# Kernel tuning notes

Measured on AMD Instinct MI355X. Metric: run time of the kernel, lower is better.

The kernel has to match this reference:

```python
import jax, jax.numpy as jnp
import numpy as np

DIM_IN = 768
DIM_EMB = 512
DIM_ATTN = 384
N_EXPERTS = 13
TOP_K = 5
NUM_CLS = 2
K_INST = 100000  # instances per bag (WSI patches)


def setup_inputs() -> dict:
    key = jax.random.key(0)
    ks = jax.random.split(key, 10)
    s = 0.02  # weight init scale
    return {
        "X_tfl": jax.random.normal(ks[0], (1, N_EXPERTS, DIM_EMB), jnp.float32),
        "X": jax.random.normal(ks[1], (1, K_INST, DIM_IN), jnp.float32),
        # feat_proj: Linear(dim_in, dim_emb) + ReLU (end_with_fc=False, eval -> no dropout)
        "W_proj": (jax.random.normal(ks[2], (DIM_IN, DIM_EMB), jnp.float32) * s),
        "b_proj": jnp.zeros((DIM_EMB,), jnp.float32),
        # Attn_Net: Linear(L,D) -> Tanh -> Linear(D,1)
        "W_attn1": (jax.random.normal(ks[3], (DIM_EMB, DIM_ATTN), jnp.float32) * s),
        "b_attn1": jnp.zeros((DIM_ATTN,), jnp.float32),
        "W_attn2": (jax.random.normal(ks[4], (DIM_ATTN, 1), jnp.float32) * s),
        "b_attn2": jnp.zeros((1,), jnp.float32),
        # router: Linear(dim_emb, n_experts, bias=False)
        "W_router": (jax.random.normal(ks[5], (DIM_EMB, N_EXPERTS), jnp.float32) * s),
        # pred_head: Linear(dim_emb, num_cls)
        "W_pred": (jax.random.normal(ks[6], (DIM_EMB, NUM_CLS), jnp.float32) * s),
        "b_pred": jnp.zeros((NUM_CLS,), jnp.float32),
    }


def reference(X_tfl, X, W_proj, b_proj, W_attn1, b_attn1, W_attn2, b_attn2,
              W_router, W_pred, b_pred):
    # feat_proj (eval mode: dropout is identity)
    H = jax.nn.relu(jnp.einsum('bkc,cd->bkd', X, W_proj) + b_proj)  # [1,K,512]
    # attention pooling (Attn_Net): tanh MLP -> scalar score per instance
    scores = jnp.einsum('bkd,de->bke', jnp.tanh(H @ W_attn1 + b_attn1), W_attn2) + b_attn2  # [1,K,1]
    A = jax.nn.softmax(scores[..., 0], axis=-1)      # [1,K]
    M = jnp.einsum('bk,bkd->bd', A, H)               # [1,512] slide representation
    # router + top-k gating
    router_logits = M @ W_router                     # [1,13]
    probs = jax.nn.softmax(router_logits, axis=-1)
    weights, sel_idx = jax.lax.top_k(probs, TOP_K)   # [1,5], [1,5]
    # Identity experts: expert i output is X_tfl[0, i, :]; gather selected, weighted combine
    sel = X_tfl[0][sel_idx[0]]                       # [5,512]
    moe_output = jnp.sum(weights[0][:, None] * sel, axis=0)[None, :]  # [1,512]
    logit = moe_output @ W_pred + b_pred             # [1,2]
    return logit
```

## Files before the change

### kernel.cpp

```cpp
#include <hip/hip_runtime.h>
#include <hip/hip_bf16.h>

typedef __attribute__((ext_vector_type(8))) short short8_t;
typedef __attribute__((ext_vector_type(4))) float f32x4;
typedef __attribute__((ext_vector_type(4))) unsigned int u32x4;

#define KINST 100000
#define KPAD  100096
#define DIMIN 768
#define DIMEMB 512
#define DIMATTN 384

__device__ __forceinline__ unsigned short f2bf(float f) {
    unsigned int u = __builtin_bit_cast(unsigned int, f);
    u = u + 0x7FFFu + ((u >> 16) & 1u);
    return (unsigned short)(u >> 16);
}
__device__ __forceinline__ unsigned int packbf(float a, float b) {
    return (unsigned int)f2bf(a) | ((unsigned int)f2bf(b) << 16);
}
__device__ __forceinline__ float bf2f(unsigned short h) {
    unsigned int u = ((unsigned int)h) << 16;
    return __builtin_bit_cast(float, u);
}
__device__ __forceinline__ float fast_tanh(float x) {
    const float e2 = __expf(2.f * x);
    return (e2 - 1.f) * __builtin_amdgcn_rcpf(e2 + 1.f);
}
__device__ __forceinline__ void gll16(const unsigned short* g, unsigned short* l) {
    __builtin_amdgcn_global_load_lds(
        (const __attribute__((address_space(1))) unsigned int*)g,
        (__attribute__((address_space(3))) unsigned int*)l, 16, 0, 0);
}

__global__ __launch_bounds__(256) void k_prep(
    const float* __restrict__ Wproj, const float* __restrict__ W1,
    unsigned short* __restrict__ WpTt, unsigned short* __restrict__ W1Ts)
{
    const int idx = blockIdx.x * 256 + threadIdx.x;
    if (idx < 49152) {
        const int t = idx >> 11, r = idx & 2047;
        const int n = r >> 2, c = r & 3;
        short8_t v;
        #pragma unroll
        for (int e = 0; e < 8; ++e)
            v[e] = (short)f2bf(Wproj[(size_t)(t * 32 + c * 8 + e) * DIMEMB + n]);
        *(short8_t*)&WpTt[t * 16384 + n * 32 + c * 8] = v;
    } else {
        const int j = idx - 49152;
        const int t = j / 3072, r = j % 3072;
        const int c = r / 384, n = r % 384;
        short8_t v;
        #pragma unroll
        for (int e = 0; e < 8; ++e)
            v[e] = (short)f2bf(W1[(size_t)(t * 64 + c * 8 + e) * DIMATTN + n]);
        *(short8_t*)&W1Ts[t * 24576 + n * 64 + ((c ^ (n & 7)) << 3)] = v;
    }
}

__global__ __launch_bounds__(256, 2) void k_gemm1(
    const float* __restrict__ X,
    const unsigned short* __restrict__ WpTt,
    const float* __restrict__ bproj,
    unsigned short* __restrict__ H)
{
    __shared__ unsigned short As[2][2048];
    const int tid = threadIdx.x;
    const int lane = tid & 63, w = tid >> 6;
    const int g = lane >> 4, fr = lane & 15;
    const int brow = blockIdx.x * 64;

    const int arow = tid >> 2, aq4 = tid & 3;
    int agr = brow + arow; if (agr >= KINST) agr = KINST - 1;
    const float* xsrc = X + (size_t)agr * DIMIN + aq4 * 8;
    const int awoff = arow * 32 + ((aq4 ^ ((arow >> 1) & 3)) << 3);
    const int aro = (g ^ ((fr >> 1) & 3)) << 3;

    const unsigned short* gB = WpTt + (size_t)(w * 128 + fr) * 32 + g * 8;

    f32x4 acc[4][8] = {};
    short8_t Bf[2][8];
    float4 xva, xvb;

    {
        float4 xa = *(const float4*)(xsrc);
        float4 xb = *(const float4*)(xsrc + 4);
        #pragma unroll
        for (int j = 0; j < 8; ++j)
            Bf[0][j] = *(const short8_t*)(gB + j * 512);
        xva = *(const float4*)(xsrc + 32);
        xvb = *(const float4*)(xsrc + 36);
        u32x4 p;
        p[0] = packbf(xa.x, xa.y); p[1] = packbf(xa.z, xa.w);
        p[2] = packbf(xb.x, xb.y); p[3] = packbf(xb.z, xb.w);
        *(u32x4*)&As[0][awoff] = p;
    }
    asm volatile("s_waitcnt lgkmcnt(0)" ::: "memory");
    __builtin_amdgcn_sched_barrier(0);
    __builtin_amdgcn_s_barrier();
    __builtin_amdgcn_sched_barrier(0);

#define G1STEP(P, T)                                                           \
    {                                                                          \
        if ((T) < 23) {       \
            const unsigned short* gBt = gB + (size_t)((T) + 1) * 16384;        \
            _Pragma("unroll")                                                  \
            for (int j = 0; j < 8; ++j)                                        \
                Bf[(P) ^ 1][j] = *(const short8_t*)(gBt + j * 512);            \
        }                                                                      \
        short8_t af[4];                      \
        _Pragma("unroll")                                                      \
        for (int i = 0; i < 4; ++i)                                            \
            af[i] = *(const short8_t*)&As[P][(i * 16 + fr) * 32 + aro];        \
        if ((T) < 23) {                     \
            u32x4 p;                                                           \
            p[0] = packbf(xva.x, xva.y); p[1] = packbf(xva.z, xva.w);          \
            p[2] = packbf(xvb.x, xvb.y); p[3] = packbf(xvb.z, xvb.w);          \
            *(u32x4*)&As[(P) ^ 1][awoff] = p;                                  \
        }                                                                      \
        if ((T) < 22) {                   \
            xva = *(const float4*)(xsrc + ((T) + 2) * 32);                     \
            xvb = *(const float4*)(xsrc + ((T) + 2) * 32 + 4);                 \
        }                                                                      \
        asm volatile("s_waitcnt lgkmcnt(0)" ::: "memory");                     \
        __builtin_amdgcn_sched_barrier(0);                                     \
        __builtin_amdgcn_s_barrier();                                          \
        __builtin_amdgcn_sched_barrier(0);                                     \
        __builtin_amdgcn_s_setprio(1);                                        \
        _Pragma("unroll")                                                      \
        for (int j = 0; j < 8; ++j)                                            \
            _Pragma("unroll")                                                  \
            for (int i = 0; i < 4; ++i)                                        \
                acc[i][j] = __builtin_amdgcn_mfma_f32_16x16x32_bf16(           \
                    af[i], Bf[P][j], acc[i][j], 0, 0, 0);                      \
        __builtin_amdgcn_s_setprio(0);                                        \
    }

    for (int tt = 0; tt < 24; tt += 2) {
        G1STEP(0, tt);
        G1STEP(1, tt + 1);
    }
#undef G1STEP

    #pragma unroll
    for (int j = 0; j < 8; ++j) {
        const int col = w * 128 + j * 16 + fr;
        const float bias = bproj[col];
        const int tile = (col >> 6) << 6, cc = (col >> 3) & 7, lo = col & 7;
        #pragma unroll
        for (int i = 0; i < 4; ++i) {
            const int rb = brow + i * 16 + g * 4;
            #pragma unroll
            for (int r = 0; r < 4; ++r) {
                const int row = rb + r;
                const float v = fmaxf(acc[i][j][r] + bias, 0.f);
                H[(size_t)row * DIMEMB + tile + ((cc ^ (row & 7)) << 3) + lo] =
                    (row < KINST) ? f2bf(v) : (unsigned short)0;
            }
        }
    }
}

__global__ __launch_bounds__(256) void k_gemm2(
    const unsigned short* __restrict__ H,
    const unsigned short* __restrict__ W1Ts,
    const float* __restrict__ b1,
    const float* __restrict__ W2,
    float* __restrict__ Tpart)
{
    __shared__ unsigned short As[2][8192];
    __shared__ unsigned short Bs[2][8192];
    __shared__ float sred[2][128];
    const int tid = threadIdx.x;
    const int lane = tid & 63, w = tid >> 6;
    const int wr = w >> 1, wc = w & 1;
    const int g = lane >> 4, fr = lane & 15;
    const int cb = blockIdx.x;
    const int brow = blockIdx.y * 128;
    const int bcol = cb * 128;

    const unsigned short* gA = H + (size_t)(brow + w * 32 + (lane >> 3)) * DIMEMB + (lane & 7) * 8;
    const unsigned short* gB = W1Ts + (size_t)(bcol + w * 32 + (lane >> 3)) * 64 + (lane & 7) * 8;
    const int loff = w * 2048 + lane * 8;

    f32x4 acc[4][4] = {};

    #pragma unroll
    for (int q = 0; q < 4; ++q) {
        gll16(gA + q * 4096, &As[0][loff + q * 512]);
        gll16(gB + q * 512,  &Bs[0][loff + q * 512]);
    }
    __syncthreads();

    for (int t = 0; t < 8; ++t) {
        const int buf = t & 1;
        if (t < 7) {
            #pragma unroll
            for (int q = 0; q < 4; ++q) {
                gll16(gA + (t + 1) * 64 + q * 4096,           &As[buf ^ 1][loff + q * 512]);
                gll16(gB + (size_t)(t + 1) * 24576 + q * 512, &Bs[buf ^ 1][loff + q * 512]);
            }
        }
        __builtin_amdgcn_s_setprio(1);
        #pragma unroll
        for (int kk = 0; kk < 2; ++kk) {
            short8_t af[4];
            #pragma unroll
            for (int i = 0; i < 4; ++i) {
                const int row = wr * 64 + i * 16 + fr;
                af[i] = *(const short8_t*)&As[buf][row * 64 + (((kk * 4 + g) ^ (fr & 7)) << 3)];
            }
            #pragma unroll
            for (int j = 0; j < 4; ++j) {
                const int rowb = wc * 64 + j * 16 + fr;
                const short8_t bf = *(const short8_t*)&Bs[buf][rowb * 64 + (((kk * 4 + g) ^ (fr & 7)) << 3)];
                #pragma unroll
                for (int i = 0; i < 4; ++i)
                    acc[i][j] = __builtin_amdgcn_mfma_f32_16x16x32_bf16(af[i], bf, acc[i][j], 0, 0, 0);
            }
        }
        __builtin_amdgcn_s_setprio(0);
        if (t < 7) __syncthreads();
    }

    float ps[4][4] = {};
    #pragma unroll
    for (int j = 0; j < 4; ++j) {
        const int col = bcol + wc * 64 + j * 16 + fr;
        const float bb = b1[col], ww = W2[col];
        #pragma unroll
        for (int i = 0; i < 4; ++i)
            #pragma unroll
            for (int r = 0; r < 4; ++r)
                ps[i][r] += fast_tanh(acc[i][j][r] + bb) * ww;
    }
    #pragma unroll
    for (int off = 1; off < 16; off <<= 1)
        #pragma unroll
        for (int i = 0; i < 4; ++i)
            #pragma unroll
            for (int r = 0; r < 4; ++r)
                ps[i][r] += __shfl_xor(ps[i][r], off, 64);
    if (fr == 0) {
        #pragma unroll
        for (int i = 0; i < 4; ++i)
            #pragma unroll
            for (int r = 0; r < 4; ++r)
                sred[wc][wr * 64 + i * 16 + g * 4 + r] = ps[i][r];
    }
    __syncthreads();
    if (tid < 128)
        Tpart[(size_t)cb * KPAD + brow + tid] = sred[0][tid] + sred[1][tid];
}

__global__ __launch_bounds__(512) void k_poolE(
    const float* __restrict__ Tpart,
    const unsigned short* __restrict__ H,
    const float* __restrict__ b2,
    float* __restrict__ Spart,
    float* __restrict__ Mpart)
{
    __shared__ float Elds[1024];
    __shared__ float red[8][512];
    __shared__ float ssum[8];
    const int tid = threadIdx.x, lane = tid & 63, w = tid >> 6;
    const int base = blockIdx.x * 1024;
    const float bb = b2[0];
    float es = 0.f;
    #pragma unroll
    for (int u = 0; u < 2; ++u) {
        const int r = base + u * 512 + tid;
        float e = 0.f;
        if (r < KINST)
            e = __expf(Tpart[r] + Tpart[KPAD + r] + Tpart[2 * KPAD + r] + bb);
        Elds[u * 512 + tid] = e;
        es += e;
    }
    #pragma unroll
    for (int off = 1; off < 64; off <<= 1) es += __shfl_xor(es, off, 64);
    if (lane == 0) ssum[w] = es;
    __syncthreads();
    if (tid == 0) {
        float t = 0.f;
        #pragma unroll
        for (int i = 0; i < 8; ++i) t += ssum[i];
        Spart[blockIdx.x] = t;
    }

    float pa[8] = {};
    const int tile = (lane >> 3) << 6, cf = lane & 7;
    for (int i = 0; i < 128; ++i) {
        const int lr = i * 8 + w;
        const float e = Elds[lr];
        if (e != 0.f) {
            const int r = base + lr;
            const short8_t v = *(const short8_t*)(H + (size_t)r * DIMEMB + tile + ((cf ^ (r & 7)) << 3));
            #pragma unroll
            for (int j = 0; j < 8; ++j) pa[j] += e * bf2f((unsigned short)v[j]);
        }
    }
    #pragma unroll
    for (int j = 0; j < 8; ++j) red[w][lane * 8 + j] = pa[j];
    __syncthreads();
    float s2 = 0.f;
    #pragma unroll
    for (int k = 0; k < 8; ++k) s2 += red[k][tid];
    Mpart[(size_t)blockIdx.x * DIMEMB + tid] = s2;
}

__global__ __launch_bounds__(512) void k_head(
    const float* __restrict__ Spart,
    const float* __restrict__ Mpart,
    const float* __restrict__ Wr,
    const float* __restrict__ Xtfl,
    const float* __restrict__ Wp,
    const float* __restrict__ bp,
    float* __restrict__ outp)
{
    __shared__ float Mlds[512];
    __shared__ float logits[13];
    __shared__ float wsel[5];
    __shared__ int isel[5];
    __shared__ float Slds;
    __shared__ float swred[8];
    __shared__ float r0s[8], r1s[8];
    const int tid = threadIdx.x, lane = tid & 63, w = tid >> 6;

    float s = 0.f;
    if (tid < 98) s = Spart[tid];
    #pragma unroll
    for (int off = 1; off < 64; off <<= 1) s += __shfl_xor(s, off, 64);
    if (lane == 0) swred[w] = s;

    float m = 0.f;
    #pragma unroll 2
    for (int b = 0; b < 98; ++b) m += Mpart[(size_t)b * 512 + tid];

    __syncthreads();
    if (tid == 0) {
        float t = 0.f;
        #pragma unroll
        for (int i = 0; i < 8; ++i) t += swred[i];
        Slds = t;
    }
    __syncthreads();
    Mlds[tid] = m / Slds;
    __syncthreads();
    if (tid < 13) {
        float l = 0.f;
        for (int dd = 0; dd < 512; ++dd) l += Mlds[dd] * Wr[dd * 13 + tid];
        logits[tid] = l;
    }
    __syncthreads();
    if (tid == 0) {
        float mx = -1e30f;
        for (int i = 0; i < 13; ++i) mx = fmaxf(mx, logits[i]);
        float pe[13]; float sum = 0.f;
        for (int i = 0; i < 13; ++i) { pe[i] = __expf(logits[i] - mx); sum += pe[i]; }
        unsigned used = 0;
        for (int t = 0; t < 5; ++t) {
            int bi = 0; float bv = -1.f;
            for (int i = 0; i < 13; ++i)
                if (!((used >> i) & 1u) && pe[i] > bv) { bv = pe[i]; bi = i; }
            used |= (1u << bi);
            wsel[t] = bv / sum;
            isel[t] = bi;
        }
    }
    __syncthreads();
    float mo = 0.f;
    #pragma unroll
    for (int t = 0; t < 5; ++t) mo += wsel[t] * Xtfl[isel[t] * 512 + tid];
    float p0 = mo * Wp[tid * 2 + 0];
    float p1 = mo * Wp[tid * 2 + 1];
    #pragma unroll
    for (int off = 1; off < 64; off <<= 1) {
        p0 += __shfl_xor(p0, off, 64);
        p1 += __shfl_xor(p1, off, 64);
    }
    if (lane == 0) { r0s[w] = p0; r1s[w] = p1; }
    __syncthreads();
    if (tid == 0) {
        float a = bp[0], b = bp[1];
        for (int i = 0; i < 8; ++i) { a += r0s[i]; b += r1s[i]; }
        outp[0] = a; outp[1] = b;
    }
}

extern "C" void kernel_launch(void* const* d_in, const int* in_sizes, int n_in,
                              void* d_out, int out_size, void* d_ws, size_t ws_size,
                              hipStream_t stream)
{
    const float* Xtfl  = (const float*)d_in[0];
    const float* X     = (const float*)d_in[1];
    const float* Wproj = (const float*)d_in[2];
    const float* bproj = (const float*)d_in[3];
    const float* W1    = (const float*)d_in[4];
    const float* b1    = (const float*)d_in[5];
    const float* W2    = (const float*)d_in[6];
    const float* b2    = (const float*)d_in[7];
    const float* Wr    = (const float*)d_in[8];
    const float* Wp    = (const float*)d_in[9];
    const float* bp    = (const float*)d_in[10];
    float* out = (float*)d_out;

    char* ws = (char*)d_ws;
    size_t off = 0;
    unsigned short* H    = (unsigned short*)(ws + off); off += (size_t)KPAD * DIMEMB * 2;
    unsigned short* WpTt = (unsigned short*)(ws + off); off += (size_t)DIMEMB * DIMIN * 2;
    unsigned short* W1Ts = (unsigned short*)(ws + off); off += (size_t)DIMATTN * DIMEMB * 2;
    float* Tpart = (float*)(ws + off); off += (size_t)3 * KPAD * 4;
    float* Spart = (float*)(ws + off); off += 1024;
    float* Mpart = (float*)(ws + off); off += (size_t)98 * DIMEMB * 4;

    k_prep<<<288, 256, 0, stream>>>(Wproj, W1, WpTt, W1Ts);
    k_gemm1<<<1564, 256, 0, stream>>>(X, WpTt, bproj, H);
    k_gemm2<<<dim3(3, 782), 256, 0, stream>>>(H, W1Ts, b1, W2, Tpart);
    k_poolE<<<98, 512, 0, stream>>>(Tpart, H, b2, Spart, Mpart);
    k_head<<<1, 512, 0, stream>>>(Spart, Mpart, Wr, Xtfl, Wp, bp, out);
}
```

Before: 329.1 us.

## Split gemm1 across two column blocks with 128-deep K tiles and occupancy 3

Restructures the projection GEMM so each block computes a 64x256 output tile (grid now 2x1564) with K steps of 128 instead of 32. This cuts the number of barriers from 24 to 6 per block and halves accumulator registers, which allows a launch bound of 3 blocks per CU. Weights are relaid out in 128-wide K chunks and loaded straight into registers in four sub-steps, interleaved with the MFMAs. The trade-off is that each X row tile is now read and converted to bf16 twice, once per column block, which adds global traffic on the largest input.

```diff
diff --git a/kernel.cpp b/kernel.cpp
--- a/kernel.cpp
+++ b/kernel.cpp
@@ -4,6 +4,7 @@
 typedef __attribute__((ext_vector_type(8))) short short8_t;
 typedef __attribute__((ext_vector_type(4))) float f32x4;
 typedef __attribute__((ext_vector_type(4))) unsigned int u32x4;
+typedef __attribute__((ext_vector_type(2))) unsigned int u32x2;
 
 #define KINST 100000
 #define KPAD  100096
@@ -35,17 +36,17 @@
 
 __global__ __launch_bounds__(256) void k_prep(
     const float* __restrict__ Wproj, const float* __restrict__ W1,
-    unsigned short* __restrict__ WpTt, unsigned short* __restrict__ W1Ts)
+    unsigned short* __restrict__ WpT6, unsigned short* __restrict__ W1Ts)
 {
     const int idx = blockIdx.x * 256 + threadIdx.x;
     if (idx < 49152) {
-        const int t = idx >> 11, r = idx & 2047;
-        const int n = r >> 2, c = r & 3;
+        const int t = idx >> 13, r = idx & 8191;
+        const int n = r >> 4, kc = r & 15;
         short8_t v;
         #pragma unroll
         for (int e = 0; e < 8; ++e)
-            v[e] = (short)f2bf(Wproj[(size_t)(t * 32 + c * 8 + e) * DIMEMB + n]);
-        *(short8_t*)&WpTt[t * 16384 + n * 32 + c * 8] = v;
+            v[e] = (short)f2bf(Wproj[(size_t)(t * 128 + kc * 8 + e) * DIMEMB + n]);
+        *(short8_t*)&WpT6[((size_t)(t * 512 + n) * 16 + kc) * 8] = v;
     } else {
         const int j = idx - 49152;
         const int t = j / 3072, r = j % 3072;
@@ -58,42 +59,55 @@
     }
 }
 
-__global__ __launch_bounds__(256, 2) void k_gemm1(
+__global__ __launch_bounds__(256, 3) void k_gemm1(
     const float* __restrict__ X,
-    const unsigned short* __restrict__ WpTt,
+    const unsigned short* __restrict__ WpT6,
     const float* __restrict__ bproj,
     unsigned short* __restrict__ H)
 {
-    __shared__ unsigned short As[2][2048];
+    __shared__ unsigned short As[2][8192];
     const int tid = threadIdx.x;
     const int lane = tid & 63, w = tid >> 6;
     const int g = lane >> 4, fr = lane & 15;
-    const int brow = blockIdx.x * 64;
-
-    const int arow = tid >> 2, aq4 = tid & 3;
-    int agr = brow + arow; if (agr >= KINST) agr = KINST - 1;
-    const float* xsrc = X + (size_t)agr * DIMIN + aq4 * 8;
-    const int awoff = arow * 32 + ((aq4 ^ ((arow >> 1) & 3)) << 3);
-    const int aro = (g ^ ((fr >> 1) & 3)) << 3;
-
-    const unsigned short* gB = WpTt + (size_t)(w * 128 + fr) * 32 + g * 8;
-
-    f32x4 acc[4][8] = {};
-    short8_t Bf[2][8];
-    float4 xva, xvb;
+    const int bcol = blockIdx.x * 256;
+    const int brow = blockIdx.y * 64;
+
+    const int arow0 = tid >> 5;
+    const int akk  = (tid * 4) & 127;
+    const int aw0  = arow0 * 128 + ((((tid >> 1) & 15) ^ (arow0 & 7)) << 3) + (tid & 1) * 4;
+    int gofs[8];
+    #pragma unroll
+    for (int q = 0; q < 8; ++q) {
+        int grow = brow + q * 8 + arow0;
+        if (grow >= KINST) grow = KINST - 1;
+        gofs[q] = grow * DIMIN + akk;
+    }
+
+    const unsigned short* gB = WpT6 + (size_t)(bcol + w * 64 + fr) * 128 + g * 8;
+    const int xk = (fr & 7);
+
+    f32x4 acc[4][4] = {};
+    float4 xvA[4], xvB[4];
 
     {
-        float4 xa = *(const float4*)(xsrc);
-        float4 xb = *(const float4*)(xsrc + 4);
-        #pragma unroll
-        for (int j = 0; j < 8; ++j)
-            Bf[0][j] = *(const short8_t*)(gB + j * 512);
-        xva = *(const float4*)(xsrc + 32);
-        xvb = *(const float4*)(xsrc + 36);
-        u32x4 p;
-        p[0] = packbf(xa.x, xa.y); p[1] = packbf(xa.z, xa.w);
-        p[2] = packbf(xb.x, xb.y); p[3] = packbf(xb.z, xb.w);
-        *(u32x4*)&As[0][awoff] = p;
+        #pragma unroll
+        for (int q = 0; q < 4; ++q) xvA[q] = *(const float4*)(X + gofs[q]);
+        #pragma unroll
+        for (int q = 0; q < 4; ++q) xvB[q] = *(const float4*)(X + gofs[q + 4]);
+        #pragma unroll
+        for (int q = 0; q < 4; ++q) {
+            u32x2 p; p[0] = packbf(xvA[q].x, xvA[q].y); p[1] = packbf(xvA[q].z, xvA[q].w);
+            *(u32x2*)&As[0][aw0 + q * 1024] = p;
+        }
+        #pragma unroll
+        for (int q = 0; q < 4; ++q) {
+            u32x2 p; p[0] = packbf(xvB[q].x, xvB[q].y); p[1] = packbf(xvB[q].z, xvB[q].w);
+            *(u32x2*)&As[0][aw0 + (q + 4) * 1024] = p;
+        }
+        #pragma unroll
+        for (int q = 0; q < 4; ++q) xvA[q] = *(const float4*)(X + gofs[q] + 128);
+        #pragma unroll
+        for (int q = 0; q < 4; ++q) xvB[q] = *(const float4*)(X + gofs[q + 4] + 128);
     }
     asm volatile("s_waitcnt lgkmcnt(0)" ::: "memory");
     __builtin_amdgcn_sched_barrier(0);
@@ -102,60 +116,112 @@
 
 #define G1STEP(P, T)                                                           \
     {                                                                          \
-        if ((T) < 23) {       \
-            const unsigned short* gBt = gB + (size_t)((T) + 1) * 16384;        \
-            _Pragma("unroll")                                                  \
-            for (int j = 0; j < 8; ++j)                                        \
-                Bf[(P) ^ 1][j] = *(const short8_t*)(gBt + j * 512);            \
+        const unsigned short* gBt = gB + (size_t)(T) * 65536;                  \
+        short8_t B0[4], B1[4], B2[4], B3[4];                                   \
+        _Pragma("unroll")                                                      \
+        for (int j = 0; j < 4; ++j) B0[j] = *(const short8_t*)(gBt + j * 2048);\
+        _Pragma("unroll")                                                      \
+        for (int j = 0; j < 4; ++j) B1[j] = *(const short8_t*)(gBt + j * 2048 + 32); \
+        if ((T) < 5) {          \
+            _Pragma("unroll")                                                  \
+            for (int q = 0; q < 4; ++q) {                                      \
+                u32x2 p; p[0] = packbf(xvA[q].x, xvA[q].y);                    \
+                p[1] = packbf(xvA[q].z, xvA[q].w);                             \
+                *(u32x2*)&As[(P) ^ 1][aw0 + q * 1024] = p;                     \
+            }                                                                  \
+            _Pragma("unroll")                                                  \
+            for (int q = 0; q < 4; ++q) {                                      \
+                u32x2 p; p[0] = packbf(xvB[q].x, xvB[q].y);                    \
+                p[1] = packbf(xvB[q].z, xvB[q].w);                             \
+                *(u32x2*)&As[(P) ^ 1][aw0 + (q + 4) * 1024] = p;               \
+            }                                                                  \
         }                                                                      \
-        short8_t af[4];                      \
+        if ((T) < 4) {                    \
+            _Pragma("unroll")                                                  \
+            for (int q = 0; q < 4; ++q)                                        \
+                xvA[q] = *(const float4*)(X + gofs[q] + ((T) + 2) * 128);      \
+            _Pragma("unroll")                                                  \
+            for (int q = 0; q < 4; ++q)                                        \
+                xvB[q] = *(const float4*)(X + gofs[q + 4] + ((T) + 2) * 128);  \
+        }                                                                      \
+        short8_t af[4];                                                        \
+                                                                  \
         _Pragma("unroll")                                                      \
         for (int i = 0; i < 4; ++i)                                            \
-            af[i] = *(const short8_t*)&As[P][(i * 16 + fr) * 32 + aro];        \
-        if ((T) < 23) {                     \
-            u32x4 p;                                                           \
-            p[0] = packbf(xva.x, xva.y); p[1] = packbf(xva.z, xva.w);          \
-            p[2] = packbf(xvb.x, xvb.y); p[3] = packbf(xvb.z, xvb.w);          \
-            *(u32x4*)&As[(P) ^ 1][awoff] = p;                                  \
+            af[i] = *(const short8_t*)&As[P][(i * 16 + fr) * 128 + (((0 + g) ^ xk) << 3)]; \
+        _Pragma("unroll")                                                      \
+        for (int j = 0; j < 4; ++j) B2[j] = *(const short8_t*)(gBt + j * 2048 + 64); \
+        __builtin_amdgcn_s_setprio(1);                                        \
+        _Pragma("unroll")                                                      \
+        for (int j = 0; j < 4; ++j)                                            \
+            _Pragma("unroll")                                                  \
+            for (int i = 0; i < 4; ++i)                                        \
+                acc[i][j] = __builtin_amdgcn_mfma_f32_16x16x32_bf16(af[i], B0[j], acc[i][j], 0, 0, 0); \
+        __builtin_amdgcn_s_setprio(0);                                        \
+                                                                  \
+        _Pragma("unroll")                                                      \
+        for (int i = 0; i < 4; ++i)                                            \
+            af[i] = *(const short8_t*)&As[P][(i * 16 + fr) * 128 + (((4 + g) ^ xk) << 3)]; \
+        _Pragma("unroll")                                                      \
+        for (int j = 0; j < 4; ++j) B3[j] = *(const short8_t*)(gBt + j * 2048 + 96); \
+        __builtin_amdgcn_s_setprio(1);                                        \
+        _Pragma("unroll")                                                      \
+        for (int j = 0; j < 4; ++j)                                            \
+            _Pragma("unroll")                                                  \
+            for (int i = 0; i < 4; ++i)                                        \
+                acc[i][j] = __builtin_amdgcn_mfma_f32_16x16x32_bf16(af[i], B1[j], acc[i][j], 0, 0, 0); \
+        __builtin_amdgcn_s_setprio(0);                                        \
+                                                                  \
+        _Pragma("unroll")                                                      \
+        for (int i = 0; i < 4; ++i)                                            \
+            af[i] = *(const short8_t*)&As[P][(i * 16 + fr) * 128 + (((8 + g) ^ xk) << 3)]; \
+        __builtin_amdgcn_s_setprio(1);                                        \
+        _Pragma("unroll")                                                      \
+        for (int j = 0; j < 4; ++j)                                            \
+            _Pragma("unroll")                                                  \
+            for (int i = 0; i < 4; ++i)                                        \
+                acc[i][j] = __builtin_amdgcn_mfma_f32_16x16x32_bf16(af[i], B2[j], acc[i][j], 0, 0, 0); \
+        __builtin_amdgcn_s_setprio(0);                                        \
+                                                                  \
+        _Pragma("unroll")                                                      \
+        for (int i = 0; i < 4; ++i)                                            \
+            af[i] = *(const short8_t*)&As[P][(i * 16 + fr) * 128 + (((12 + g) ^ xk) << 3)]; \
+        __builtin_amdgcn_s_setprio(1);                                        \
+        _Pragma("unroll")                                                      \
+        for (int j = 0; j < 4; ++j)                                            \
+            _Pragma("unroll")                                                  \
+            for (int i = 0; i < 4; ++i)                                        \
+                acc[i][j] = __builtin_amdgcn_mfma_f32_16x16x32_bf16(af[i], B3[j], acc[i][j], 0, 0, 0); \
+        __builtin_amdgcn_s_setprio(0);                                        \
+        if ((T) < 5) {                                                         \
+            asm volatile("s_waitcnt lgkmcnt(0)" ::: "memory");                 \
+            __builtin_amdgcn_sched_barrier(0);                                 \
+            __builtin_amdgcn_s_barrier();                                      \
+            __builtin_amdgcn_sched_barrier(0);                                 \
         }                                                                      \
-        if ((T) < 22) {                   \
-            xva = *(const float4*)(xsrc + ((T) + 2) * 32);                     \
-            xvb = *(const float4*)(xsrc + ((T) + 2) * 32 + 4);                 \
-        }                                                                      \
-        asm volatile("s_waitcnt lgkmcnt(0)" ::: "memory");                     \
-        __builtin_amdgcn_sched_barrier(0);                                     \
-        __builtin_amdgcn_s_barrier();                                          \
-        __builtin_amdgcn_sched_barrier(0);                                     \
-        __builtin_amdgcn_s_setprio(1);                                        \
-        _Pragma("unroll")                                                      \
-        for (int j = 0; j < 8; ++j)                                            \
-            _Pragma("unroll")                                                  \
-            for (int i = 0; i < 4; ++i)                                        \
-                acc[i][j] = __builtin_amdgcn_mfma_f32_16x16x32_bf16(           \
-                    af[i], Bf[P][j], acc[i][j], 0, 0, 0);                      \
-        __builtin_amdgcn_s_setprio(0);                                        \
-    }
-
-    for (int tt = 0; tt < 24; tt += 2) {
-        G1STEP(0, tt);
-        G1STEP(1, tt + 1);
-    }
+    }
+
+    G1STEP(0, 0)
+    G1STEP(1, 1)
+    G1STEP(0, 2)
+    G1STEP(1, 3)
+    G1STEP(0, 4)
+    G1STEP(1, 5)
 #undef G1STEP
 
     #pragma unroll
-    for (int j = 0; j < 8; ++j) {
-        const int col = w * 128 + j * 16 + fr;
+    for (int j = 0; j < 4; ++j) {
+        const int col = bcol + w * 64 + j * 16 + fr;
         const float bias = bproj[col];
         const int tile = (col >> 6) << 6, cc = (col >> 3) & 7, lo = col & 7;
         #pragma unroll
         for (int i = 0; i < 4; ++i) {
-            const int rb = brow + i * 16 + g * 4;
             #pragma unroll
             for (int r = 0; r < 4; ++r) {
-                const int row = rb + r;
+                const int grow = brow + i * 16 + g * 4 + r;
                 const float v = fmaxf(acc[i][j][r] + bias, 0.f);
-                H[(size_t)row * DIMEMB + tile + ((cc ^ (row & 7)) << 3) + lo] =
-                    (row < KINST) ? f2bf(v) : (unsigned short)0;
+                H[(size_t)grow * DIMEMB + tile + ((cc ^ (grow & 7)) << 3) + lo] =
+                    (grow < KINST) ? f2bf(v) : (unsigned short)0;
             }
         }
     }
@@ -407,14 +473,14 @@
     char* ws = (char*)d_ws;
     size_t off = 0;
     unsigned short* H    = (unsigned short*)(ws + off); off += (size_t)KPAD * DIMEMB * 2;
-    unsigned short* WpTt = (unsigned short*)(ws + off); off += (size_t)DIMEMB * DIMIN * 2;
+    unsigned short* WpT6 = (unsigned short*)(ws + off); off += (size_t)DIMEMB * DIMIN * 2;
     unsigned short* W1Ts = (unsigned short*)(ws + off); off += (size_t)DIMATTN * DIMEMB * 2;
     float* Tpart = (float*)(ws + off); off += (size_t)3 * KPAD * 4;
     float* Spart = (float*)(ws + off); off += 1024;
     float* Mpart = (float*)(ws + off); off += (size_t)98 * DIMEMB * 4;
 
-    k_prep<<<288, 256, 0, stream>>>(Wproj, W1, WpTt, W1Ts);
-    k_gemm1<<<1564, 256, 0, stream>>>(X, WpTt, bproj, H);
+    k_prep<<<288, 256, 0, stream>>>(Wproj, W1, WpT6, W1Ts);
+    k_gemm1<<<dim3(2, 1564), 256, 0, stream>>>(X, WpT6, bproj, H);
     k_gemm2<<<dim3(3, 782), 256, 0, stream>>>(H, W1Ts, b1, W2, Tpart);
     k_poolE<<<98, 512, 0, stream>>>(Tpart, H, b2, Spart, Mpart);
     k_head<<<1, 512, 0, stream>>>(Spart, Mpart, Wr, Xtfl, Wp, bp, out);
```

Result: slower. 449.4 us (median of 2 runs) (+36.6%).

## Split gemm1 into single-wave blocks over a column-by-row grid, removing barriers

Applied to the files above, without the earlier changes.

Each k_gemm1 block now holds a single 64-thread wave that computes a 64x128 output tile. The grid becomes 4 column blocks by 1564 row blocks, so the wave loads and converts its own copy of the X tile into LDS and no workgroup barriers are needed. The register double-buffering of the B fragments is dropped: B is loaded in the same step it is used. In exchange, X is read and converted to bf16 four times instead of once, so the kernel relies on L2 hits from neighbouring column blocks. The B load latency is also now exposed within each step.

```diff
diff --git a/kernel.cpp b/kernel.cpp
--- a/kernel.cpp
+++ b/kernel.cpp
@@ -4,6 +4,7 @@
 typedef __attribute__((ext_vector_type(8))) short short8_t;
 typedef __attribute__((ext_vector_type(4))) float f32x4;
 typedef __attribute__((ext_vector_type(4))) unsigned int u32x4;
+typedef __attribute__((ext_vector_type(2))) unsigned int u32x2;
 
 #define KINST 100000
 #define KPAD  100096
@@ -58,104 +59,101 @@
     }
 }
 
-__global__ __launch_bounds__(256, 2) void k_gemm1(
+__global__ __launch_bounds__(64, 2) void k_gemm1(
     const float* __restrict__ X,
     const unsigned short* __restrict__ WpTt,
     const float* __restrict__ bproj,
     unsigned short* __restrict__ H)
 {
     __shared__ unsigned short As[2][2048];
-    const int tid = threadIdx.x;
-    const int lane = tid & 63, w = tid >> 6;
+    const int lane = threadIdx.x;
     const int g = lane >> 4, fr = lane & 15;
-    const int brow = blockIdx.x * 64;
-
-    const int arow = tid >> 2, aq4 = tid & 3;
-    int agr = brow + arow; if (agr >= KINST) agr = KINST - 1;
-    const float* xsrc = X + (size_t)agr * DIMIN + aq4 * 8;
-    const int awoff = arow * 32 + ((aq4 ^ ((arow >> 1) & 3)) << 3);
+    const int bcol = blockIdx.x * 128;
+    const int brow = blockIdx.y * 64;
+
+    const int srow = lane >> 3;
+    const int sc4  = (lane & 7) * 4;
+    const int c2   = (lane & 7) >> 1;
+    const int half = (lane & 1) * 4;
+    int gofs[8], awof[8];
+    #pragma unroll
+    for (int q = 0; q < 8; ++q) {
+        int grow = brow + q * 8 + srow;
+        if (grow >= KINST) grow = KINST - 1;
+        gofs[q] = grow * DIMIN + sc4;
+        const int row = q * 8 + srow;
+        awof[q] = row * 32 + ((c2 ^ ((row >> 1) & 3)) << 3) + half;
+    }
     const int aro = (g ^ ((fr >> 1) & 3)) << 3;
 
-    const unsigned short* gB = WpTt + (size_t)(w * 128 + fr) * 32 + g * 8;
+    const unsigned short* gB = WpTt + (size_t)(bcol + fr) * 32 + g * 8;
 
     f32x4 acc[4][8] = {};
-    short8_t Bf[2][8];
-    float4 xva, xvb;
-
-    {
-        float4 xa = *(const float4*)(xsrc);
-        float4 xb = *(const float4*)(xsrc + 4);
-        #pragma unroll
-        for (int j = 0; j < 8; ++j)
-            Bf[0][j] = *(const short8_t*)(gB + j * 512);
-        xva = *(const float4*)(xsrc + 32);
-        xvb = *(const float4*)(xsrc + 36);
-        u32x4 p;
-        p[0] = packbf(xa.x, xa.y); p[1] = packbf(xa.z, xa.w);
-        p[2] = packbf(xb.x, xb.y); p[3] = packbf(xb.z, xb.w);
-        *(u32x4*)&As[0][awoff] = p;
-    }
-    asm volatile("s_waitcnt lgkmcnt(0)" ::: "memory");
-    __builtin_amdgcn_sched_barrier(0);
-    __builtin_amdgcn_s_barrier();
-    __builtin_amdgcn_sched_barrier(0);
+    float4 xv[8];
+
+    #pragma unroll
+    for (int q = 0; q < 8; ++q) xv[q] = *(const float4*)(X + gofs[q]);
+    #pragma unroll
+    for (int q = 0; q < 8; ++q) {
+        u32x2 p; p[0] = packbf(xv[q].x, xv[q].y); p[1] = packbf(xv[q].z, xv[q].w);
+        *(u32x2*)&As[0][awof[q]] = p;
+    }
+    #pragma unroll
+    for (int q = 0; q < 8; ++q) xv[q] = *(const float4*)(X + gofs[q] + 32);
 
 #define G1STEP(P, T)                                                           \
     {                                                                          \
-        if ((T) < 23) {       \
-            const unsigned short* gBt = gB + (size_t)((T) + 1) * 16384;        \
+        short8_t Bf[8];                                                        \
+        const unsigned short* gBt = gB + (size_t)(T) * 16384;                  \
+        _Pragma("unroll")                                                      \
+        for (int j = 0; j < 8; ++j)                                            \
+            Bf[j] = *(const short8_t*)(gBt + j * 512);                         \
+        if ((T) < 23) {               \
             _Pragma("unroll")                                                  \
-            for (int j = 0; j < 8; ++j)                                        \
-                Bf[(P) ^ 1][j] = *(const short8_t*)(gBt + j * 512);            \
+            for (int q = 0; q < 8; ++q) {                                      \
+                u32x2 p; p[0] = packbf(xv[q].x, xv[q].y);                      \
+                p[1] = packbf(xv[q].z, xv[q].w);                               \
+                *(u32x2*)&As[(P) ^ 1][awof[q]] = p;                            \
+            }                                                                  \
         }                                                                      \
-        short8_t af[4];                      \
+        if ((T) < 22) {             \
+            _Pragma("unroll")                                                  \
+            for (int q = 0; q < 8; ++q)                                        \
+                xv[q] = *(const float4*)(X + gofs[q] + ((T) + 2) * 32);        \
+        }                                                                      \
+        short8_t af[4];                                                        \
         _Pragma("unroll")                                                      \
         for (int i = 0; i < 4; ++i)                                            \
             af[i] = *(const short8_t*)&As[P][(i * 16 + fr) * 32 + aro];        \
-        if ((T) < 23) {                     \
-            u32x4 p;                                                           \
-            p[0] = packbf(xva.x, xva.y); p[1] = packbf(xva.z, xva.w);          \
-            p[2] = packbf(xvb.x, xvb.y); p[3] = packbf(xvb.z, xvb.w);          \
-            *(u32x4*)&As[(P) ^ 1][awoff] = p;                                  \
-        }                                                                      \
-        if ((T) < 22) {                   \
-            xva = *(const float4*)(xsrc + ((T) + 2) * 32);                     \
-            xvb = *(const float4*)(xsrc + ((T) + 2) * 32 + 4);                 \
-        }                                                                      \
-        asm volatile("s_waitcnt lgkmcnt(0)" ::: "memory");                     \
-        __builtin_amdgcn_sched_barrier(0);                                     \
-        __builtin_amdgcn_s_barrier();                                          \
-        __builtin_amdgcn_sched_barrier(0);                                     \
         __builtin_amdgcn_s_setprio(1);                                        \
         _Pragma("unroll")                                                      \
         for (int j = 0; j < 8; ++j)                                            \
             _Pragma("unroll")                                                  \
             for (int i = 0; i < 4; ++i)                                        \
                 acc[i][j] = __builtin_amdgcn_mfma_f32_16x16x32_bf16(           \
-                    af[i], Bf[P][j], acc[i][j], 0, 0, 0);                      \
+                    af[i], Bf[j], acc[i][j], 0, 0, 0);                         \
         __builtin_amdgcn_s_setprio(0);                                        \
     }
 
-    for (int tt = 0; tt < 24; tt += 2) {
-        G1STEP(0, tt);
-        G1STEP(1, tt + 1);
+    for (int t2 = 0; t2 < 24; t2 += 2) {
+        G1STEP(0, t2)
+        G1STEP(1, t2 + 1)
     }
 #undef G1STEP
 
     #pragma unroll
     for (int j = 0; j < 8; ++j) {
-        const int col = w * 128 + j * 16 + fr;
+        const int col = bcol + j * 16 + fr;
         const float bias = bproj[col];
         const int tile = (col >> 6) << 6, cc = (col >> 3) & 7, lo = col & 7;
         #pragma unroll
         for (int i = 0; i < 4; ++i) {
-            const int rb = brow + i * 16 + g * 4;
             #pragma unroll
             for (int r = 0; r < 4; ++r) {
-                const int row = rb + r;
+                const int grow = brow + i * 16 + g * 4 + r;
                 const float v = fmaxf(acc[i][j][r] + bias, 0.f);
-                H[(size_t)row * DIMEMB + tile + ((cc ^ (row & 7)) << 3) + lo] =
-                    (row < KINST) ? f2bf(v) : (unsigned short)0;
+                H[(size_t)grow * DIMEMB + tile + ((cc ^ (grow & 7)) << 3) + lo] =
+                    (grow < KINST) ? f2bf(v) : (unsigned short)0;
             }
         }
     }
@@ -414,7 +412,7 @@
     float* Mpart = (float*)(ws + off); off += (size_t)98 * DIMEMB * 4;
 
     k_prep<<<288, 256, 0, stream>>>(Wproj, W1, WpTt, W1Ts);
-    k_gemm1<<<1564, 256, 0, stream>>>(X, WpTt, bproj, H);
+    k_gemm1<<<dim3(4, 1564), 64, 0, stream>>>(X, WpTt, bproj, H);
     k_gemm2<<<dim3(3, 782), 256, 0, stream>>>(H, W1Ts, b1, W2, Tpart);
     k_poolE<<<98, 512, 0, stream>>>(Tpart, H, b2, Spart, Mpart);
     k_head<<<1, 512, 0, stream>>>(Spart, Mpart, Wr, Xtfl, Wp, bp, out);
```

Result: slower. 384.1 us (+16.7%).
